# Kernel optimization log

Hardware: AMD Instinct MI355X
Metric: run time of the kernel (lower is better)

Reference implementation:

```python
import jax, jax.numpy as jnp
import numpy as np

B, N, Q, K = 8, 1024, 128, 16  # batch, surface points, query points, d_embedding


def _layer_norm(x, w, b, eps=1e-5):
    m = x.mean(-1, keepdims=True)
    v = ((x - m) ** 2).mean(-1, keepdims=True)
    return (x - m) * jax.lax.rsqrt(v + eps) * w + b


def _positional_embedding(coords, pe_log_scale, k):
    # coords: [..., 2] -> [..., k]; layout [sin(x/d_i), cos(x/d_i), sin(y/d_i), cos(y/d_i)]
    num = k // 4
    div = jnp.exp(pe_log_scale) ** (4.0 * jnp.arange(num, dtype=jnp.float32) / k)  # [num]
    x = coords[..., 0:1] / div  # [..., num]
    y = coords[..., 1:2] / div
    pe = jnp.stack([jnp.sin(x), jnp.cos(x), jnp.sin(y), jnp.cos(y)], axis=-1)  # [..., num, 4]
    return pe.reshape(coords.shape[:-1] + (k,))


def setup_inputs() -> dict:
    key = jax.random.key(0)
    ks = jax.random.split(key, 8)
    return {
        'lm_s': jax.random.normal(ks[0], (B, N), jnp.float32),
        'ttm_s': jax.random.uniform(ks[1], (B, N), jnp.float32),
        'tv_s': jax.random.uniform(ks[2], (B, N), jnp.float32) + 0.05,
        'lm_q': jax.random.normal(ks[3], (B, Q), jnp.float32),
        'ttm_q': jax.random.uniform(ks[4], (B, Q), jnp.float32),
        # learned params
        'log_scale_kernels': 0.1 * jax.random.normal(ks[5], (K, 2), jnp.float32),  # per-kernel elliptical log scales
        'ln_s_w': jnp.ones((K,), jnp.float32),
        'ln_s_b': jnp.zeros((K,), jnp.float32),
        'ln_q_w': jnp.ones((K,), jnp.float32),
        'ln_q_b': jnp.zeros((K,), jnp.float32),
        'pe_log_scale': jnp.log(jnp.float32(10000.0)),
    }


def reference(lm_s, ttm_s, tv_s, lm_q, ttm_q,
              log_scale_kernels, ln_s_w, ln_s_b, ln_q_w, ln_q_b, pe_log_scale):
    k = log_scale_kernels.shape[0]
    # bandwidth_i = erfinv(i/(K+1)) * sqrt(2), i = 1..K
    i = jnp.arange(1, k + 1, dtype=jnp.float32)
    bw = jax.scipy.special.erfinv(i / (k + 1)) * jnp.sqrt(jnp.float32(2.0))  # [K]

    coords_s = jnp.stack([lm_s, ttm_s], axis=-1)   # [B,N,2]
    coords_q = jnp.stack([lm_q, ttm_q], axis=-1)   # [B,Q,2]
    all_coords = jnp.concatenate([coords_s, coords_q], axis=1)  # [B,M,2], M=N+Q

    # pairwise squared differences to surface points
    diff2 = (all_coords[:, :, None, :] - coords_s[:, None, :, :]) ** 2  # [B,M,N,2]

    scale = jnp.exp(log_scale_kernels)        # [K,2]
    tr = scale.sum(-1)                         # [K]
    # normalized elliptical distances per kernel
    nd = jnp.einsum('bmnc,kc->bkmn', diff2, scale) / tr[None, :, None, None]
    kern = jnp.exp(-nd / (2.0 * bw ** 2)[None, :, None, None])  # [B,K,M,N]

    wsum = jnp.einsum('bkmn,bn->bmk', kern, tv_s)   # [B,M,K]
    norm = kern.sum(-1).transpose(0, 2, 1)          # [B,M,K]
    emb = wsum / norm                                # [B,M,K]

    n = coords_s.shape[1]
    surf_emb = _layer_norm(emb[:, :n], ln_s_w, ln_s_b)
    query_emb = _layer_norm(emb[:, n:], ln_q_w, ln_q_b)

    sqrt2 = jnp.sqrt(jnp.float32(2.0))
    surf_out = surf_emb + _positional_embedding(coords_s, pe_log_scale, k) * sqrt2
    query_out = query_emb + _positional_embedding(coords_q, pe_log_scale, k) * sqrt2
    return jnp.concatenate([surf_out, query_out], axis=1)  # [B,M,K]
```

## Files before the change

kernel.cpp:

```cpp
#include <hip/hip_runtime.h>
#include <math.h>

namespace {
constexpr int B = 8, N = 1024, Q = 128, K = 16, M = N + Q;
constexpr int WAVES_PER_BLOCK = 4;
constexpr int NWAVES = B * M;
constexpr int NBLOCKS = NWAVES / WAVES_PER_BLOCK;
}

#if __has_builtin(__builtin_amdgcn_exp2f)
  #define EXP2F(x) __builtin_amdgcn_exp2f(x)
#else
  #define EXP2F(x) exp2f(x)
#endif

__device__ __forceinline__ float sgpr_broadcast(float x) {
  return __uint_as_float(__builtin_amdgcn_readfirstlane(__float_as_uint(x)));
}

__global__ __launch_bounds__(256, 8) void IvySPT_main(
    const float* __restrict__ lm_s, const float* __restrict__ ttm_s,
    const float* __restrict__ tv_s, const float* __restrict__ lm_q,
    const float* __restrict__ ttm_q, const float* __restrict__ lsk,
    const float* __restrict__ ln_s_w, const float* __restrict__ ln_s_b,
    const float* __restrict__ ln_q_w, const float* __restrict__ ln_q_b,
    const float* __restrict__ pls_p,
    float* __restrict__ out)
{
  __shared__ float sC[2][K];
  if (threadIdx.x < K) {
    const int k = threadIdx.x;
    float s0 = expf(lsk[2 * k + 0]);
    float s1 = expf(lsk[2 * k + 1]);
    float tr = s0 + s1;
    float x  = (float)(k + 1) / (float)(K + 1);
    float bw = erfinvf(x) * 1.41421356237309504880f;
    float denom = tr * 2.0f * bw * bw;
    const float LOG2E = 1.44269504088896340736f;
    sC[0][k] = -s0 * LOG2E / denom;
    sC[1][k] = -s1 * LOG2E / denom;
  }
  __syncthreads();

  const int lane = threadIdx.x & 63;
  const int wid  = threadIdx.x >> 6;
  const int w    = blockIdx.x * WAVES_PER_BLOCK + wid;
  const int b    = w / M;
  const int m    = w - b * M;

  float cmx, cmy;
  if (m < N) { cmx = lm_s[b * N + m];       cmy = ttm_s[b * N + m]; }
  else       { cmx = lm_q[b * Q + (m - N)]; cmy = ttm_q[b * Q + (m - N)]; }

  float cA[K], cB[K];
#pragma unroll
  for (int k = 0; k < K; k++) {
    cA[k] = sgpr_broadcast(sC[0][k]);
    cB[k] = sgpr_broadcast(sC[1][k]);
  }

  float wsum[K], nrm[K];
#pragma unroll
  for (int k = 0; k < K; k++) { wsum[k] = 0.f; nrm[k] = 0.f; }

  const float2* xs2 = (const float2*)(lm_s  + b * N);
  const float2* ys2 = (const float2*)(ttm_s + b * N);
  const float2* tv2 = (const float2*)(tv_s  + b * N);

#pragma unroll 2
  for (int i = 0; i < N / 128; i++) {
    float2 sx = xs2[i * 64 + lane];
    float2 sy = ys2[i * 64 + lane];
    float2 t  = tv2[i * 64 + lane];
    float dx0 = cmx - sx.x, dx1 = cmx - sx.y;
    float dy0 = cmy - sy.x, dy1 = cmy - sy.y;
    float dx20 = dx0 * dx0, dx21 = dx1 * dx1;
    float dy20 = dy0 * dy0, dy21 = dy1 * dy1;
#pragma unroll
    for (int k = 0; k < K; k++) {
      float a0 = fmaf(dy20, cB[k], dx20 * cA[k]);
      float a1 = fmaf(dy21, cB[k], dx21 * cA[k]);
      float e0 = EXP2F(a0);
      float e1 = EXP2F(a1);
      wsum[k] = fmaf(e0, t.x, wsum[k]);
      nrm[k] += e0;
      wsum[k] = fmaf(e1, t.y, wsum[k]);
      nrm[k] += e1;
    }
  }

  __shared__ float red[WAVES_PER_BLOCK][64][17];
  float (*rp)[17] = red[wid];
  const int col = lane & 15;
  const int qq  = lane >> 4;

  float totW, totN;
  {
#pragma unroll
    for (int c = 0; c < K; c++) rp[lane][c] = wsum[c];
    asm volatile("s_waitcnt lgkmcnt(0)" ::: "memory");
    float s = 0.f;
#pragma unroll
    for (int r = 0; r < 16; r++) s += rp[qq * 16 + r][col];
    asm volatile("s_waitcnt lgkmcnt(0)" ::: "memory");
    s += __shfl_xor(s, 16);
    s += __shfl_xor(s, 32);
    totW = s;
  }
  {
#pragma unroll
    for (int c = 0; c < K; c++) rp[lane][c] = nrm[c];
    asm volatile("s_waitcnt lgkmcnt(0)" ::: "memory");
    float s = 0.f;
#pragma unroll
    for (int r = 0; r < 16; r++) s += rp[qq * 16 + r][col];
    s += __shfl_xor(s, 16);
    s += __shfl_xor(s, 32);
    totN = s;
  }

  float emb = totW / totN;

  float s1 = emb;
  s1 += __shfl_xor(s1, 1); s1 += __shfl_xor(s1, 2);
  s1 += __shfl_xor(s1, 4); s1 += __shfl_xor(s1, 8);
  float mean = s1 * (1.f / 16.f);
  float dv = emb - mean;
  float s2 = dv * dv;
  s2 += __shfl_xor(s2, 1); s2 += __shfl_xor(s2, 2);
  s2 += __shfl_xor(s2, 4); s2 += __shfl_xor(s2, 8);
  float inv = rsqrtf(s2 * (1.f / 16.f) + 1e-5f);

  const int k = col;
  float lw, lb;
  if (m < N) { lw = ln_s_w[k]; lb = ln_s_b[k]; }
  else       { lw = ln_q_w[k]; lb = ln_q_b[k]; }
  float normed = dv * inv * lw + lb;

  float pls = pls_p[0];
  float invdiv = expf(-pls * (float)(k >> 2) * 0.25f);
  float cv  = (k & 2) ? cmy : cmx;
  float arg = cv * invdiv;
  float pe  = (k & 1) ? cosf(arg) : sinf(arg);
  float val = fmaf(pe, 1.41421356237309504880f, normed);

  if (lane < 16) out[((size_t)(b * M + m)) * K + k] = val;
}

extern "C" void kernel_launch(void* const* d_in, const int* in_sizes, int n_in,
                              void* d_out, int out_size, void* d_ws, size_t ws_size,
                              hipStream_t stream) {
  const float* lm_s   = (const float*)d_in[0];
  const float* ttm_s  = (const float*)d_in[1];
  const float* tv_s   = (const float*)d_in[2];
  const float* lm_q   = (const float*)d_in[3];
  const float* ttm_q  = (const float*)d_in[4];
  const float* lsk    = (const float*)d_in[5];
  const float* ln_s_w = (const float*)d_in[6];
  const float* ln_s_b = (const float*)d_in[7];
  const float* ln_q_w = (const float*)d_in[8];
  const float* ln_q_b = (const float*)d_in[9];
  const float* pls    = (const float*)d_in[10];

  float* out = (float*)d_out;

  hipLaunchKernelGGL(IvySPT_main, dim3(NBLOCKS), dim3(256), 0, stream,
                     lm_s, ttm_s, tv_s, lm_q, ttm_q, lsk,
                     ln_s_w, ln_s_b, ln_q_w, ln_q_b, pls, out);
}
```

Measured before the change: 32.73 us.

## Offload kernel-weighted reductions to bf16 MFMA with hi/lo split

```diff
diff --git a/kernel.cpp b/kernel.cpp
--- a/kernel.cpp
+++ b/kernel.cpp
@@ -1,24 +1,32 @@
 #include <hip/hip_runtime.h>
 #include <math.h>
 
+typedef float  f32x4  __attribute__((ext_vector_type(4)));
+typedef short  bf16x8 __attribute__((ext_vector_type(8)));
+typedef unsigned int u32x4 __attribute__((ext_vector_type(4)));
+
 namespace {
-constexpr int B = 8, N = 1024, Q = 128, K = 16, M = N + Q;
-constexpr int WAVES_PER_BLOCK = 4;
-constexpr int NWAVES = B * M;
-constexpr int NBLOCKS = NWAVES / WAVES_PER_BLOCK;
-}
-
-#if __has_builtin(__builtin_amdgcn_exp2f)
-  #define EXP2F(x) __builtin_amdgcn_exp2f(x)
-#else
-  #define EXP2F(x) exp2f(x)
-#endif
-
-__device__ __forceinline__ float sgpr_broadcast(float x) {
+constexpr int B = 8, N = 1024, Qn = 128, K = 16, M = N + Qn;
+constexpr int GROUPS = M / 16;
+constexpr int NBLK   = B * GROUPS;
+constexpr int WPB    = 8;
+constexpr int SLICE  = N / WPB;
+constexpr int CHUNKS = SLICE / 32;
+}
+
+#define EXP2F(x) __builtin_amdgcn_exp2f(x)
+
+__device__ __forceinline__ unsigned pack_trunc(float a, float b) {
+  return (__float_as_uint(a) >> 16) | (__float_as_uint(b) & 0xFFFF0000u);
+}
+__device__ __forceinline__ float hi_part(float x) {
+  return __uint_as_float(__float_as_uint(x) & 0xFFFF0000u);
+}
+__device__ __forceinline__ float sgpr_bc(float x) {
   return __uint_as_float(__builtin_amdgcn_readfirstlane(__float_as_uint(x)));
 }
 
-__global__ __launch_bounds__(256, 8) void IvySPT_main(
+__global__ __launch_bounds__(512) void IvySPT_main(
     const float* __restrict__ lm_s, const float* __restrict__ ttm_s,
     const float* __restrict__ tv_s, const float* __restrict__ lm_q,
     const float* __restrict__ ttm_q, const float* __restrict__ lsk,
@@ -28,6 +36,8 @@
     float* __restrict__ out)
 {
   __shared__ float sC[2][K];
+  __shared__ float sRed[WPB][16][2 * K + 1];
+
   if (threadIdx.x < K) {
     const int k = threadIdx.x;
     float s0 = expf(lsk[2 * k + 0]);
@@ -42,109 +52,156 @@
   }
   __syncthreads();
 
-  const int lane = threadIdx.x & 63;
-  const int wid  = threadIdx.x >> 6;
-  const int w    = blockIdx.x * WAVES_PER_BLOCK + wid;
-  const int b    = w / M;
-  const int m    = w - b * M;
-
-  float cmx, cmy;
-  if (m < N) { cmx = lm_s[b * N + m];       cmy = ttm_s[b * N + m]; }
-  else       { cmx = lm_q[b * Q + (m - N)]; cmy = ttm_q[b * Q + (m - N)]; }
+  const int l  = threadIdx.x & 63;
+  const int w  = threadIdx.x >> 6;
+  const int b  = blockIdx.x / GROUPS;
+  const int g  = blockIdx.x % GROUPS;
+  const int mi = l & 15;
+  const int jc = l >> 4;
+
+  const int mg = g * 16 + mi;
+  float xm, ym;
+  if (g < 64) { xm = lm_s[b * N + mg];        ym = ttm_s[b * N + mg]; }
+  else        { xm = lm_q[b * Qn + (mg - N)]; ym = ttm_q[b * Qn + (mg - N)]; }
 
   float cA[K], cB[K];
 #pragma unroll
-  for (int k = 0; k < K; k++) {
-    cA[k] = sgpr_broadcast(sC[0][k]);
-    cB[k] = sgpr_broadcast(sC[1][k]);
-  }
-
-  float wsum[K], nrm[K];
-#pragma unroll
-  for (int k = 0; k < K; k++) { wsum[k] = 0.f; nrm[k] = 0.f; }
-
-  const float2* xs2 = (const float2*)(lm_s  + b * N);
-  const float2* ys2 = (const float2*)(ttm_s + b * N);
-  const float2* tv2 = (const float2*)(tv_s  + b * N);
-
-#pragma unroll 2
-  for (int i = 0; i < N / 128; i++) {
-    float2 sx = xs2[i * 64 + lane];
-    float2 sy = ys2[i * 64 + lane];
-    float2 t  = tv2[i * 64 + lane];
-    float dx0 = cmx - sx.x, dx1 = cmx - sx.y;
-    float dy0 = cmy - sy.x, dy1 = cmy - sy.y;
-    float dx20 = dx0 * dx0, dx21 = dx1 * dx1;
-    float dy20 = dy0 * dy0, dy21 = dy1 * dy1;
+  for (int k = 0; k < K; k++) { cA[k] = sgpr_bc(sC[0][k]); cB[k] = sgpr_bc(sC[1][k]); }
+
+  f32x4 acc[K];
+#pragma unroll
+  for (int k = 0; k < K; k++) acc[k] = f32x4{0.f, 0.f, 0.f, 0.f};
+
+  const float* xs = lm_s  + b * N;
+  const float* ys = ttm_s + b * N;
+  const float* tv = tv_s  + b * N;
+
+#pragma unroll 1
+  for (int c = 0; c < CHUNKS; ++c) {
+    const int nb = w * SLICE + c * 32 + jc * 8;
+    float4 x0 = *(const float4*)(xs + nb);
+    float4 x1 = *(const float4*)(xs + nb + 4);
+    float4 y0 = *(const float4*)(ys + nb);
+    float4 y1 = *(const float4*)(ys + nb + 4);
+    float4 t0 = *(const float4*)(tv + nb);
+    float4 t1 = *(const float4*)(tv + nb + 4);
+
+    float dx2[8], dy2[8];
+    {
+      float d;
+      d = xm - x0.x; dx2[0] = d * d;  d = xm - x0.y; dx2[1] = d * d;
+      d = xm - x0.z; dx2[2] = d * d;  d = xm - x0.w; dx2[3] = d * d;
+      d = xm - x1.x; dx2[4] = d * d;  d = xm - x1.y; dx2[5] = d * d;
+      d = xm - x1.z; dx2[6] = d * d;  d = xm - x1.w; dx2[7] = d * d;
+      d = ym - y0.x; dy2[0] = d * d;  d = ym - y0.y; dy2[1] = d * d;
+      d = ym - y0.z; dy2[2] = d * d;  d = ym - y0.w; dy2[3] = d * d;
+      d = ym - y1.x; dy2[4] = d * d;  d = ym - y1.y; dy2[5] = d * d;
+      d = ym - y1.z; dy2[6] = d * d;  d = ym - y1.w; dy2[7] = d * d;
+    }
+
+    u32x4 afh, afl;
+    {
+      unsigned th0 = pack_trunc(t0.x, t0.y);
+      unsigned th1 = pack_trunc(t0.z, t0.w);
+      unsigned th2 = pack_trunc(t1.x, t1.y);
+      unsigned th3 = pack_trunc(t1.z, t1.w);
+      float tl0 = t0.x - hi_part(t0.x), tl1 = t0.y - hi_part(t0.y);
+      float tl2 = t0.z - hi_part(t0.z), tl3 = t0.w - hi_part(t0.w);
+      float tl4 = t1.x - hi_part(t1.x), tl5 = t1.y - hi_part(t1.y);
+      float tl6 = t1.z - hi_part(t1.z), tl7 = t1.w - hi_part(t1.w);
+      unsigned tq0 = pack_trunc(tl0, tl1);
+      unsigned tq1 = pack_trunc(tl2, tl3);
+      unsigned tq2 = pack_trunc(tl4, tl5);
+      unsigned tq3 = pack_trunc(tl6, tl7);
+      const unsigned ones = 0x3F803F80u;
+      afh.x = (mi == 0) ? th0 : ((mi == 1) ? tq0 : ((mi == 2) ? ones : 0u));
+      afh.y = (mi == 0) ? th1 : ((mi == 1) ? tq1 : ((mi == 2) ? ones : 0u));
+      afh.z = (mi == 0) ? th2 : ((mi == 1) ? tq2 : ((mi == 2) ? ones : 0u));
+      afh.w = (mi == 0) ? th3 : ((mi == 1) ? tq3 : ((mi == 2) ? ones : 0u));
+    }
+    bf16x8 A = __builtin_bit_cast(bf16x8, afh);
+    (void)afl;
+
 #pragma unroll
     for (int k = 0; k < K; k++) {
-      float a0 = fmaf(dy20, cB[k], dx20 * cA[k]);
-      float a1 = fmaf(dy21, cB[k], dx21 * cA[k]);
-      float e0 = EXP2F(a0);
-      float e1 = EXP2F(a1);
-      wsum[k] = fmaf(e0, t.x, wsum[k]);
-      nrm[k] += e0;
-      wsum[k] = fmaf(e1, t.y, wsum[k]);
-      nrm[k] += e1;
-    }
-  }
-
-  __shared__ float red[WAVES_PER_BLOCK][64][17];
-  float (*rp)[17] = red[wid];
-  const int col = lane & 15;
-  const int qq  = lane >> 4;
-
-  float totW, totN;
-  {
-#pragma unroll
-    for (int c = 0; c < K; c++) rp[lane][c] = wsum[c];
-    asm volatile("s_waitcnt lgkmcnt(0)" ::: "memory");
-    float s = 0.f;
-#pragma unroll
-    for (int r = 0; r < 16; r++) s += rp[qq * 16 + r][col];
-    asm volatile("s_waitcnt lgkmcnt(0)" ::: "memory");
-    s += __shfl_xor(s, 16);
-    s += __shfl_xor(s, 32);
-    totW = s;
-  }
-  {
-#pragma unroll
-    for (int c = 0; c < K; c++) rp[lane][c] = nrm[c];
-    asm volatile("s_waitcnt lgkmcnt(0)" ::: "memory");
-    float s = 0.f;
-#pragma unroll
-    for (int r = 0; r < 16; r++) s += rp[qq * 16 + r][col];
-    s += __shfl_xor(s, 16);
-    s += __shfl_xor(s, 32);
-    totN = s;
-  }
-
-  float emb = totW / totN;
-
-  float s1 = emb;
-  s1 += __shfl_xor(s1, 1); s1 += __shfl_xor(s1, 2);
-  s1 += __shfl_xor(s1, 4); s1 += __shfl_xor(s1, 8);
-  float mean = s1 * (1.f / 16.f);
-  float dv = emb - mean;
-  float s2 = dv * dv;
-  s2 += __shfl_xor(s2, 1); s2 += __shfl_xor(s2, 2);
-  s2 += __shfl_xor(s2, 4); s2 += __shfl_xor(s2, 8);
-  float inv = rsqrtf(s2 * (1.f / 16.f) + 1e-5f);
-
-  const int k = col;
-  float lw, lb;
-  if (m < N) { lw = ln_s_w[k]; lb = ln_s_b[k]; }
-  else       { lw = ln_q_w[k]; lb = ln_q_b[k]; }
-  float normed = dv * inv * lw + lb;
-
-  float pls = pls_p[0];
-  float invdiv = expf(-pls * (float)(k >> 2) * 0.25f);
-  float cv  = (k & 2) ? cmy : cmx;
-  float arg = cv * invdiv;
-  float pe  = (k & 1) ? cosf(arg) : sinf(arg);
-  float val = fmaf(pe, 1.41421356237309504880f, normed);
-
-  if (lane < 16) out[((size_t)(b * M + m)) * K + k] = val;
+      float e0 = EXP2F(fmaf(dy2[0], cB[k], dx2[0] * cA[k]));
+      float e1 = EXP2F(fmaf(dy2[1], cB[k], dx2[1] * cA[k]));
+      float e2 = EXP2F(fmaf(dy2[2], cB[k], dx2[2] * cA[k]));
+      float e3 = EXP2F(fmaf(dy2[3], cB[k], dx2[3] * cA[k]));
+      float e4 = EXP2F(fmaf(dy2[4], cB[k], dx2[4] * cA[k]));
+      float e5 = EXP2F(fmaf(dy2[5], cB[k], dx2[5] * cA[k]));
+      float e6 = EXP2F(fmaf(dy2[6], cB[k], dx2[6] * cA[k]));
+      float e7 = EXP2F(fmaf(dy2[7], cB[k], dx2[7] * cA[k]));
+      u32x4 ehi, elo;
+      ehi.x = pack_trunc(e0, e1);
+      ehi.y = pack_trunc(e2, e3);
+      ehi.z = pack_trunc(e4, e5);
+      ehi.w = pack_trunc(e6, e7);
+      float l0 = e0 - hi_part(e0), l1 = e1 - hi_part(e1);
+      float l2 = e2 - hi_part(e2), l3 = e3 - hi_part(e3);
+      float l4 = e4 - hi_part(e4), l5 = e5 - hi_part(e5);
+      float l6 = e6 - hi_part(e6), l7 = e7 - hi_part(e7);
+      elo.x = pack_trunc(l0, l1);
+      elo.y = pack_trunc(l2, l3);
+      elo.z = pack_trunc(l4, l5);
+      elo.w = pack_trunc(l6, l7);
+      bf16x8 Eh = __builtin_bit_cast(bf16x8, ehi);
+      bf16x8 El = __builtin_bit_cast(bf16x8, elo);
+      acc[k] = __builtin_amdgcn_mfma_f32_16x16x32_bf16(A, Eh, acc[k], 0, 0, 0);
+      acc[k] = __builtin_amdgcn_mfma_f32_16x16x32_bf16(A, El, acc[k], 0, 0, 0);
+    }
+  }
+
+  if (l < 16) {
+#pragma unroll
+    for (int k = 0; k < K; k++) {
+      sRed[w][l][2 * k]     = acc[k].x + acc[k].y;
+      sRed[w][l][2 * k + 1] = acc[k].z;
+    }
+  }
+  __syncthreads();
+
+  if (threadIdx.x < 256) {
+    const int kk = threadIdx.x & 15;
+    const int m  = threadIdx.x >> 4;
+    float sw = 0.f, sn = 0.f;
+#pragma unroll
+    for (int ww = 0; ww < WPB; ww++) {
+      sw += sRed[ww][m][2 * kk];
+      sn += sRed[ww][m][2 * kk + 1];
+    }
+    float emb = sw / sn;
+
+    float s1 = emb;
+    s1 += __shfl_xor(s1, 1); s1 += __shfl_xor(s1, 2);
+    s1 += __shfl_xor(s1, 4); s1 += __shfl_xor(s1, 8);
+    float mean = s1 * (1.f / 16.f);
+    float dv = emb - mean;
+    float s2 = dv * dv;
+    s2 += __shfl_xor(s2, 1); s2 += __shfl_xor(s2, 2);
+    s2 += __shfl_xor(s2, 4); s2 += __shfl_xor(s2, 8);
+    float inv = rsqrtf(s2 * (1.f / 16.f) + 1e-5f);
+
+    const int row = g * 16 + m;
+    float lw, lb, cmx, cmy;
+    if (g < 64) {
+      lw = ln_s_w[kk]; lb = ln_s_b[kk];
+      cmx = lm_s[b * N + row]; cmy = ttm_s[b * N + row];
+    } else {
+      lw = ln_q_w[kk]; lb = ln_q_b[kk];
+      cmx = lm_q[b * Qn + (row - N)]; cmy = ttm_q[b * Qn + (row - N)];
+    }
+    float normed = dv * inv * lw + lb;
+
+    float pls = pls_p[0];
+    float invdiv = expf(-pls * (float)(kk >> 2) * 0.25f);
+    float cv  = (kk & 2) ? cmy : cmx;
+    float arg = cv * invdiv;
+    float pe  = (kk & 1) ? cosf(arg) : sinf(arg);
+    float val = fmaf(pe, 1.41421356237309504880f, normed);
+
+    out[((size_t)(b * M + row)) * K + kk] = val;
+  }
 }
 
 extern "C" void kernel_launch(void* const* d_in, const int* in_sizes, int n_in,
@@ -164,7 +221,7 @@
 
   float* out = (float*)d_out;
 
-  hipLaunchKernelGGL(IvySPT_main, dim3(NBLOCKS), dim3(256), 0, stream,
+  hipLaunchKernelGGL(IvySPT_main, dim3(NBLK), dim3(512), 0, stream,
                      lm_s, ttm_s, tv_s, lm_q, ttm_q, lsk,
                      ln_s_w, ln_s_b, ln_q_w, ln_q_b, pls, out);
 }
```

Measured after the change: 52.57 us. +60.6%, slower.
